# Kernel tuning notes

Hardware: AMD Instinct MI355X
Metric: run time of the kernel (lower is better)

Reference implementation:

```python
import jax, jax.numpy as jnp
import numpy as np

B, E, D = 4096, 64, 1024

def setup_inputs() -> dict:
    key = jax.random.key(0)
    k1, k2 = jax.random.split(key)
    z = jax.random.normal(k1, (B, D), dtype=jnp.float32)
    expert_keys = jax.random.normal(k2, (E, D), dtype=jnp.float32)
    log_sigma = jnp.zeros((D,), dtype=jnp.float32)
    return {"z": z, "expert_keys": expert_keys, "log_sigma": log_sigma}

def reference(z, expert_keys, log_sigma):
    # diag(sigma_inv) @ diff followed by (. * diff).sum(-1) is exactly an
    # elementwise-scaled squared distance: sum_d exp(-log_sigma_d) * diff_d^2
    sigma_inv = jnp.exp(-log_sigma)                              # [D]
    diff = z[:, None, :] - expert_keys[None, :, :]               # [B, E, D]
    mahalanobis_dist = jnp.einsum('bed,d,bed->be', diff, sigma_inv, diff)  # [B, E]
    similarity = 1.0 / (1.0 + mahalanobis_dist)                  # [B, E]
    weights = jax.nn.softmax(similarity, axis=-1)                # [B, E]
    weighted_expert = weights @ expert_keys                      # [B, D]
    return (similarity, weighted_expert)
```

## Files before the change

kernel.cpp:

```cpp
#include <hip/hip_runtime.h>
#include <hip/hip_bf16.h>

#define B_N 4096
#define E_N 64
#define D_N 1024
#define ROWS 16

typedef __bf16 bf16x8 __attribute__((ext_vector_type(8)));
typedef __bf16 bf16x4 __attribute__((ext_vector_type(4)));
typedef float f32x4 __attribute__((ext_vector_type(4)));


__global__ __launch_bounds__(256) void prep_kernel(
    const float* __restrict__ keys, const float* __restrict__ lsig,
    float* __restrict__ sinv, float* __restrict__ ak,
    __bf16* __restrict__ sk, __bf16* __restrict__ kT)
{
  __shared__ float red[4];
  __shared__ __bf16 tl[64][72];
  const int bid = blockIdx.x;
  const int t = threadIdx.x;

  if (bid < 64) {
    const int e = bid;
    const float4 k4 = *(const float4*)(keys + e * D_N + 4 * t);
    const float4 l4 = *(const float4*)(lsig + 4 * t);
    float4 s4;
    s4.x = expf(-l4.x); s4.y = expf(-l4.y); s4.z = expf(-l4.z); s4.w = expf(-l4.w);
    if (e == 0) *(float4*)(sinv + 4 * t) = s4;
    const float4 sk4 = make_float4(s4.x * k4.x, s4.y * k4.y, s4.z * k4.z, s4.w * k4.w);
    bf16x4 skb;
    skb[0] = (__bf16)sk4.x; skb[1] = (__bf16)sk4.y; skb[2] = (__bf16)sk4.z; skb[3] = (__bf16)sk4.w;
    *(bf16x4*)(sk + e * D_N + 4 * t) = skb;
    float p = sk4.x * k4.x + sk4.y * k4.y + sk4.z * k4.z + sk4.w * k4.w;
    #pragma unroll
    for (int off = 32; off > 0; off >>= 1) p += __shfl_down(p, off);
    if ((t & 63) == 0) red[t >> 6] = p;
    __syncthreads();
    if (t == 0) ak[e] = red[0] + red[1] + red[2] + red[3];
  } else {
    const int d0 = (bid - 64) * 64;
    #pragma unroll
    for (int p = 0; p < 4; ++p) {
      const int e  = p * 16 + (t >> 4);
      const int dd = (t & 15) * 4;
      const float4 k4 = *(const float4*)(keys + (size_t)e * D_N + d0 + dd);
      tl[dd + 0][e] = (__bf16)k4.x; tl[dd + 1][e] = (__bf16)k4.y;
      tl[dd + 2][e] = (__bf16)k4.z; tl[dd + 3][e] = (__bf16)k4.w;
    }
    __syncthreads();
    #pragma unroll
    for (int p = 0; p < 2; ++p) {
      const int dd = p * 32 + (t >> 3);
      const int l8 = t & 7;
      const bf16x8 v = *(const bf16x8*)&tl[dd][l8 * 8];
      *(bf16x8*)(kT + (size_t)(d0 + dd) * E_N + l8 * 8) = v;
    }
  }
}

__global__ __launch_bounds__(512) void main_kernel(
    const float* __restrict__ z, const float* __restrict__ sinv,
    const float* __restrict__ ak, const __bf16* __restrict__ sk,
    const __bf16* __restrict__ kT,
    float* __restrict__ out_sim, float* __restrict__ out_we)
{
  constexpr int ZS = D_N + 8;
  __shared__ __bf16 zlds[ROWS * ZS];
  __shared__ float azs[ROWS];
  __shared__ float pacc[4][16][17];
  __shared__ float simb[ROWS][68];
  __shared__ __bf16 wlds[ROWS][72];

  const int t  = threadIdx.x;
  const int b0 = blockIdx.x * ROWS;

  const int wave = t >> 6;
  const int lane = t & 63;
  const int ln = lane & 15;
  const int q  = lane >> 4;
  const int et = wave & 3;
  const int kh = wave >> 2;

  const float akv = ak[et * 16 + ln];

  const int sr = t >> 5;
  const int sc = t & 31;
  const float* zrow = z + (size_t)(b0 + sr) * D_N;
  float az = 0.f;
  #pragma unroll
  for (int l = 0; l < 8; ++l) {
    const int c = sc * 4 + l * 128;
    const float4 z4 = *(const float4*)(zrow + c);
    const float4 s4 = *(const float4*)(sinv + c);
    az += s4.x * z4.x * z4.x + s4.y * z4.y * z4.y + s4.z * z4.z * z4.z + s4.w * z4.w * z4.w;
    bf16x4 zb;
    zb[0] = (__bf16)z4.x; zb[1] = (__bf16)z4.y; zb[2] = (__bf16)z4.z; zb[3] = (__bf16)z4.w;
    *(bf16x4*)(&zlds[sr * ZS + c]) = zb;
  }
  az += __shfl_xor(az, 1);  az += __shfl_xor(az, 2);
  az += __shfl_xor(az, 4);  az += __shfl_xor(az, 8);
  az += __shfl_xor(az, 16);
  if (sc == 0) azs[sr] = az;

  const __bf16* bp = sk + (size_t)(et * 16 + ln) * D_N + kh * 512 + q * 8;
  const bf16x8 bpf0 = *(const bf16x8*)(bp);
  const bf16x8 bpf1 = *(const bf16x8*)(bp + 32);
  const bf16x8 bpf2 = *(const bf16x8*)(bp + 64);
  const bf16x8 bpf3 = *(const bf16x8*)(bp + 96);

  __syncthreads();

  const __bf16* ap = &zlds[ln * ZS + kh * 512 + q * 8];
  f32x4 acc = {0.f, 0.f, 0.f, 0.f};
  {
    const bf16x8 a0 = *(const bf16x8*)(ap);
    acc = __builtin_amdgcn_mfma_f32_16x16x32_bf16(a0, bpf0, acc, 0, 0, 0);
    const bf16x8 a1 = *(const bf16x8*)(ap + 32);
    acc = __builtin_amdgcn_mfma_f32_16x16x32_bf16(a1, bpf1, acc, 0, 0, 0);
    const bf16x8 a2 = *(const bf16x8*)(ap + 64);
    acc = __builtin_amdgcn_mfma_f32_16x16x32_bf16(a2, bpf2, acc, 0, 0, 0);
    const bf16x8 a3 = *(const bf16x8*)(ap + 96);
    acc = __builtin_amdgcn_mfma_f32_16x16x32_bf16(a3, bpf3, acc, 0, 0, 0);
  }
  #pragma unroll
  for (int ks = 4; ks < 16; ++ks) {
    const bf16x8 bfr = *(const bf16x8*)(bp + ks * 32);
    const bf16x8 afr = *(const bf16x8*)(ap + ks * 32);
    acc = __builtin_amdgcn_mfma_f32_16x16x32_bf16(afr, bfr, acc, 0, 0, 0);
  }

  if (kh) {
    #pragma unroll
    for (int i = 0; i < 4; ++i) pacc[et][q * 4 + i][ln] = acc[i];
  }

  const __bf16* kp0 = kT + (size_t)(wave * 16 + ln) * E_N + q * 8;
  const bf16x8 pb0 = *(const bf16x8*)(kp0);
  const bf16x8 pb1 = *(const bf16x8*)(kp0 + 32);

  __syncthreads();

  if (!kh) {
    #pragma unroll
    for (int i = 0; i < 4; ++i) {
      const int row = q * 4 + i;
      const float dot = acc[i] + pacc[et][row][ln];
      const float dist = azs[row] + akv - 2.0f * dot;
      simb[row][et * 16 + ln] = 1.0f / (1.0f + dist);
    }
  }
  __syncthreads();

  if (t < 256) {
    const float4 sv = *(const float4*)&simb[t >> 4][(t & 15) * 4];
    *(float4*)(out_sim + (size_t)(b0 + (t >> 4)) * E_N + (t & 15) * 4) = sv;
  }

  if (t < 64) {
    const int row = t >> 2, seg = t & 3;
    float v[16];
    #pragma unroll
    for (int i = 0; i < 16; ++i) v[i] = simb[row][seg * 16 + i];
    float mx = v[0];
    #pragma unroll
    for (int i = 1; i < 16; ++i) mx = fmaxf(mx, v[i]);
    mx = fmaxf(mx, __shfl_xor(mx, 1));
    mx = fmaxf(mx, __shfl_xor(mx, 2));
    float sum = 0.f;
    #pragma unroll
    for (int i = 0; i < 16; ++i) { v[i] = __expf(v[i] - mx); sum += v[i]; }
    sum += __shfl_xor(sum, 1);
    sum += __shfl_xor(sum, 2);
    const float inv = 1.0f / sum;
    #pragma unroll
    for (int i = 0; i < 16; ++i) wlds[row][seg * 16 + i] = (__bf16)(v[i] * inv);
  }
  __syncthreads();

  const bf16x8 a0 = *(const bf16x8*)&wlds[ln][q * 8];
  const bf16x8 a1 = *(const bf16x8*)&wlds[ln][32 + q * 8];
  #pragma unroll
  for (int i = 0; i < 8; ++i) {
    const int dt = wave + 8 * i;
    const int d0 = dt * 16;
    bf16x8 b0f, b1f;
    if (i == 0) { b0f = pb0; b1f = pb1; }
    else {
      const __bf16* kp = kT + (size_t)(d0 + ln) * E_N + q * 8;
      b0f = *(const bf16x8*)(kp);
      b1f = *(const bf16x8*)(kp + 32);
    }
    f32x4 o = {0.f, 0.f, 0.f, 0.f};
    o = __builtin_amdgcn_mfma_f32_16x16x32_bf16(a0, b0f, o, 0, 0, 0);
    o = __builtin_amdgcn_mfma_f32_16x16x32_bf16(a1, b1f, o, 0, 0, 0);
    #pragma unroll
    for (int j = 0; j < 4; ++j)
      out_we[(size_t)(b0 + q * 4 + j) * D_N + d0 + ln] = o[j];
  }
}

extern "C" void kernel_launch(void* const* d_in, const int* in_sizes, int n_in,
                              void* d_out, int out_size, void* d_ws, size_t ws_size,
                              hipStream_t stream)
{
  const float* z    = (const float*)d_in[0];
  const float* keys = (const float*)d_in[1];
  const float* ls   = (const float*)d_in[2];
  float* out_sim = (float*)d_out;
  float* out_we  = out_sim + (size_t)B_N * E_N;
  char* ws = (char*)d_ws;
  float*  sinv = (float*)(ws);
  float*  ak   = (float*)(ws + 4096);
  __bf16* sk   = (__bf16*)(ws + 4352);
  __bf16* kT   = (__bf16*)(ws + 135424);
  prep_kernel<<<80, 256, 0, stream>>>(keys, ls, sinv, ak, sk, kT);
  main_kernel<<<B_N / ROWS, 512, 0, stream>>>(z, sinv, ak, sk, kT, out_sim, out_we);
}
```

Before: 81.57 us.

## Fuse similarity epilogue with softmax across 256 threads and prefetch more key tiles

Both K-halves now write partial dot products to shared memory, and a single 256-thread phase combines them, computes similarity, writes it out, and does the softmax with 16-lane shuffles. This drops one block barrier and the simb staging buffer, and spreads the softmax over 256 threads instead of 64. It also prefetches four key-transpose tiles per wave before the barrier instead of one, and asks for two blocks per CU through launch bounds. The extra prefetch registers and the occupancy hint could cause register spills.

```diff
diff --git a/kernel.cpp b/kernel.cpp
--- a/kernel.cpp
+++ b/kernel.cpp
@@ -59,7 +59,7 @@
   }
 }
 
-__global__ __launch_bounds__(512) void main_kernel(
+__global__ __launch_bounds__(512, 2) void main_kernel(
     const float* __restrict__ z, const float* __restrict__ sinv,
     const float* __restrict__ ak, const __bf16* __restrict__ sk,
     const __bf16* __restrict__ kT,
@@ -68,8 +68,7 @@
   constexpr int ZS = D_N + 8;
   __shared__ __bf16 zlds[ROWS * ZS];
   __shared__ float azs[ROWS];
-  __shared__ float pacc[4][16][17];
-  __shared__ float simb[ROWS][68];
+  __shared__ float pacc[2][4][16][20];
   __shared__ __bf16 wlds[ROWS][72];
 
   const int t  = threadIdx.x;
@@ -82,7 +81,8 @@
   const int et = wave & 3;
   const int kh = wave >> 2;
 
-  const float akv = ak[et * 16 + ln];
+  f32x4 ak4 = {0.f, 0.f, 0.f, 0.f};
+  if (t < 256) ak4 = *(const f32x4*)(ak + (t & 15) * 4);
 
   const int sr = t >> 5;
   const int sc = t & 31;
@@ -130,51 +130,54 @@
     acc = __builtin_amdgcn_mfma_f32_16x16x32_bf16(afr, bfr, acc, 0, 0, 0);
   }
 
-  if (kh) {
-    #pragma unroll
-    for (int i = 0; i < 4; ++i) pacc[et][q * 4 + i][ln] = acc[i];
-  }
-
-  const __bf16* kp0 = kT + (size_t)(wave * 16 + ln) * E_N + q * 8;
-  const bf16x8 pb0 = *(const bf16x8*)(kp0);
-  const bf16x8 pb1 = *(const bf16x8*)(kp0 + 32);
+  #pragma unroll
+  for (int i = 0; i < 4; ++i) pacc[kh][et][q * 4 + i][ln] = acc[i];
+
+  bf16x8 pb0a, pb0b, pb1a, pb1b, pb2a, pb2b, pb3a, pb3b;
+  {
+    const __bf16* kp;
+    kp = kT + (size_t)((wave +  0) * 16 + ln) * E_N + q * 8;
+    pb0a = *(const bf16x8*)(kp); pb0b = *(const bf16x8*)(kp + 32);
+    kp = kT + (size_t)((wave +  8) * 16 + ln) * E_N + q * 8;
+    pb1a = *(const bf16x8*)(kp); pb1b = *(const bf16x8*)(kp + 32);
+    kp = kT + (size_t)((wave + 16) * 16 + ln) * E_N + q * 8;
+    pb2a = *(const bf16x8*)(kp); pb2b = *(const bf16x8*)(kp + 32);
+    kp = kT + (size_t)((wave + 24) * 16 + ln) * E_N + q * 8;
+    pb3a = *(const bf16x8*)(kp); pb3b = *(const bf16x8*)(kp + 32);
+  }
 
   __syncthreads();
 
-  if (!kh) {
-    #pragma unroll
-    for (int i = 0; i < 4; ++i) {
-      const int row = q * 4 + i;
-      const float dot = acc[i] + pacc[et][row][ln];
-      const float dist = azs[row] + akv - 2.0f * dot;
-      simb[row][et * 16 + ln] = 1.0f / (1.0f + dist);
-    }
-  }
-  __syncthreads();
-
   if (t < 256) {
-    const float4 sv = *(const float4*)&simb[t >> 4][(t & 15) * 4];
-    *(float4*)(out_sim + (size_t)(b0 + (t >> 4)) * E_N + (t & 15) * 4) = sv;
-  }
-
-  if (t < 64) {
-    const int row = t >> 2, seg = t & 3;
-    float v[16];
-    #pragma unroll
-    for (int i = 0; i < 16; ++i) v[i] = simb[row][seg * 16 + i];
-    float mx = v[0];
-    #pragma unroll
-    for (int i = 1; i < 16; ++i) mx = fmaxf(mx, v[i]);
+    const int row = t >> 4, seg = t & 15;
+    const f32x4 p0 = *(const f32x4*)&pacc[0][seg >> 2][row][(seg & 3) * 4];
+    const f32x4 p1 = *(const f32x4*)&pacc[1][seg >> 2][row][(seg & 3) * 4];
+    const float azr = azs[row];
+    f32x4 s;
+    #pragma unroll
+    for (int j = 0; j < 4; ++j) {
+      const float dist = azr + ak4[j] - 2.0f * (p0[j] + p1[j]);
+      s[j] = 1.0f / (1.0f + dist);
+    }
+    *(f32x4*)(out_sim + (size_t)(b0 + row) * E_N + seg * 4) = s;
+    float mx = fmaxf(fmaxf(s[0], s[1]), fmaxf(s[2], s[3]));
     mx = fmaxf(mx, __shfl_xor(mx, 1));
     mx = fmaxf(mx, __shfl_xor(mx, 2));
+    mx = fmaxf(mx, __shfl_xor(mx, 4));
+    mx = fmaxf(mx, __shfl_xor(mx, 8));
+    float v[4];
     float sum = 0.f;
     #pragma unroll
-    for (int i = 0; i < 16; ++i) { v[i] = __expf(v[i] - mx); sum += v[i]; }
+    for (int j = 0; j < 4; ++j) { v[j] = __expf(s[j] - mx); sum += v[j]; }
     sum += __shfl_xor(sum, 1);
     sum += __shfl_xor(sum, 2);
+    sum += __shfl_xor(sum, 4);
+    sum += __shfl_xor(sum, 8);
     const float inv = 1.0f / sum;
-    #pragma unroll
-    for (int i = 0; i < 16; ++i) wlds[row][seg * 16 + i] = (__bf16)(v[i] * inv);
+    bf16x4 wq;
+    #pragma unroll
+    for (int j = 0; j < 4; ++j) wq[j] = (__bf16)(v[j] * inv);
+    *(bf16x4*)&wlds[row][seg * 4] = wq;
   }
   __syncthreads();
 
@@ -185,7 +188,10 @@
     const int dt = wave + 8 * i;
     const int d0 = dt * 16;
     bf16x8 b0f, b1f;
-    if (i == 0) { b0f = pb0; b1f = pb1; }
+    if      (i == 0) { b0f = pb0a; b1f = pb0b; }
+    else if (i == 1) { b0f = pb1a; b1f = pb1b; }
+    else if (i == 2) { b0f = pb2a; b1f = pb2b; }
+    else if (i == 3) { b0f = pb3a; b1f = pb3b; }
     else {
       const __bf16* kp = kT + (size_t)(d0 + ln) * E_N + q * 8;
       b0f = *(const bf16x8*)(kp);
```

Result: slower. 84.45 us (+3.5%).

## Precompute bf16 z and row norms in prep kernel, load bf16 in main

Applied to the files above, without the earlier changes.

Moves the fp32-to-bf16 conversion of z and the scaled squared-norm reduction from the main kernel into extra blocks of the prep kernel, writing bf16 z and per-row norms to workspace. The main kernel then loads half as many bytes for z and skips the reduction. The exchange is an extra full write and read of a bf16 copy of z (8 MB in, 16 MB read overall), plus more prep blocks that run serially before the main kernel.

```diff
diff --git a/kernel.cpp b/kernel.cpp
--- a/kernel.cpp
+++ b/kernel.cpp
@@ -13,8 +13,10 @@
 
 __global__ __launch_bounds__(256) void prep_kernel(
     const float* __restrict__ keys, const float* __restrict__ lsig,
-    float* __restrict__ sinv, float* __restrict__ ak,
-    __bf16* __restrict__ sk, __bf16* __restrict__ kT)
+    const float* __restrict__ z,
+    float* __restrict__ az_g, float* __restrict__ ak,
+    __bf16* __restrict__ sk, __bf16* __restrict__ kT,
+    __bf16* __restrict__ zb)
 {
   __shared__ float red[4];
   __shared__ __bf16 tl[64][72];
@@ -27,7 +29,6 @@
     const float4 l4 = *(const float4*)(lsig + 4 * t);
     float4 s4;
     s4.x = expf(-l4.x); s4.y = expf(-l4.y); s4.z = expf(-l4.z); s4.w = expf(-l4.w);
-    if (e == 0) *(float4*)(sinv + 4 * t) = s4;
     const float4 sk4 = make_float4(s4.x * k4.x, s4.y * k4.y, s4.z * k4.z, s4.w * k4.w);
     bf16x4 skb;
     skb[0] = (__bf16)sk4.x; skb[1] = (__bf16)sk4.y; skb[2] = (__bf16)sk4.z; skb[3] = (__bf16)sk4.w;
@@ -38,7 +39,7 @@
     if ((t & 63) == 0) red[t >> 6] = p;
     __syncthreads();
     if (t == 0) ak[e] = red[0] + red[1] + red[2] + red[3];
-  } else {
+  } else if (bid < 80) {
     const int d0 = (bid - 64) * 64;
     #pragma unroll
     for (int p = 0; p < 4; ++p) {
@@ -56,11 +57,37 @@
       const bf16x8 v = *(const bf16x8*)&tl[dd][l8 * 8];
       *(bf16x8*)(kT + (size_t)(d0 + dd) * E_N + l8 * 8) = v;
     }
+  } else {
+    const int zr0 = (bid - 80) * 8;
+    const int zr  = t >> 5;
+    const int zc  = t & 31;
+    const float* zrow = z + (size_t)(zr0 + zr) * D_N;
+    __bf16* zorow = zb + (size_t)(zr0 + zr) * D_N;
+    float az = 0.f;
+    #pragma unroll
+    for (int l = 0; l < 8; ++l) {
+      const int c = zc * 4 + l * 128;
+      const float4 z4 = *(const float4*)(zrow + c);
+      const float4 l4 = *(const float4*)(lsig + c);
+      float4 s4;
+      s4.x = __expf(-l4.x); s4.y = __expf(-l4.y);
+      s4.z = __expf(-l4.z); s4.w = __expf(-l4.w);
+      az += s4.x * z4.x * z4.x + s4.y * z4.y * z4.y
+          + s4.z * z4.z * z4.z + s4.w * z4.w * z4.w;
+      bf16x4 zbv;
+      zbv[0] = (__bf16)z4.x; zbv[1] = (__bf16)z4.y;
+      zbv[2] = (__bf16)z4.z; zbv[3] = (__bf16)z4.w;
+      *(bf16x4*)(zorow + c) = zbv;
+    }
+    az += __shfl_xor(az, 1);  az += __shfl_xor(az, 2);
+    az += __shfl_xor(az, 4);  az += __shfl_xor(az, 8);
+    az += __shfl_xor(az, 16);
+    if (zc == 0) az_g[zr0 + zr] = az;
   }
 }
 
 __global__ __launch_bounds__(512) void main_kernel(
-    const float* __restrict__ z, const float* __restrict__ sinv,
+    const __bf16* __restrict__ zb, const float* __restrict__ az_g,
     const float* __restrict__ ak, const __bf16* __restrict__ sk,
     const __bf16* __restrict__ kT,
     float* __restrict__ out_sim, float* __restrict__ out_we)
@@ -86,22 +113,14 @@
 
   const int sr = t >> 5;
   const int sc = t & 31;
-  const float* zrow = z + (size_t)(b0 + sr) * D_N;
-  float az = 0.f;
+  const __bf16* zrow = zb + (size_t)(b0 + sr) * D_N;
   #pragma unroll
-  for (int l = 0; l < 8; ++l) {
-    const int c = sc * 4 + l * 128;
-    const float4 z4 = *(const float4*)(zrow + c);
-    const float4 s4 = *(const float4*)(sinv + c);
-    az += s4.x * z4.x * z4.x + s4.y * z4.y * z4.y + s4.z * z4.z * z4.z + s4.w * z4.w * z4.w;
-    bf16x4 zb;
-    zb[0] = (__bf16)z4.x; zb[1] = (__bf16)z4.y; zb[2] = (__bf16)z4.z; zb[3] = (__bf16)z4.w;
-    *(bf16x4*)(&zlds[sr * ZS + c]) = zb;
-  }
-  az += __shfl_xor(az, 1);  az += __shfl_xor(az, 2);
-  az += __shfl_xor(az, 4);  az += __shfl_xor(az, 8);
-  az += __shfl_xor(az, 16);
-  if (sc == 0) azs[sr] = az;
+  for (int l = 0; l < 4; ++l) {
+    const int c = sc * 8 + l * 256;
+    const bf16x8 v = *(const bf16x8*)(zrow + c);
+    *(bf16x8*)(&zlds[sr * ZS + c]) = v;
+  }
+  if (t < ROWS) azs[t] = az_g[b0 + t];
 
   const __bf16* bp = sk + (size_t)(et * 16 + ln) * D_N + kh * 512 + q * 8;
   const bf16x8 bpf0 = *(const bf16x8*)(bp);
@@ -210,10 +229,11 @@
   float* out_sim = (float*)d_out;
   float* out_we  = out_sim + (size_t)B_N * E_N;
   char* ws = (char*)d_ws;
-  float*  sinv = (float*)(ws);
-  float*  ak   = (float*)(ws + 4096);
-  __bf16* sk   = (__bf16*)(ws + 4352);
-  __bf16* kT   = (__bf16*)(ws + 135424);
-  prep_kernel<<<80, 256, 0, stream>>>(keys, ls, sinv, ak, sk, kT);
-  main_kernel<<<B_N / ROWS, 512, 0, stream>>>(z, sinv, ak, sk, kT, out_sim, out_we);
+  float*  az_g = (float*)(ws);
+  float*  ak   = (float*)(ws + 16384);
+  __bf16* sk   = (__bf16*)(ws + 16640);
+  __bf16* kT   = (__bf16*)(ws + 147712);
+  __bf16* zb   = (__bf16*)(ws + 1048576);
+  prep_kernel<<<80 + B_N / 8, 256, 0, stream>>>(keys, ls, z, az_g, ak, sk, kT, zb);
+  main_kernel<<<B_N / ROWS, 512, 0, stream>>>(zb, az_g, ak, sk, kT, out_sim, out_we);
 }
```

Measured after the change: 83.83 us. 2.8% more time.
